# Performance work log

Measured on AMD Instinct MI355X. Metric: run time of the kernel, lower is better.

The kernel has to match this reference:

```python
import jax, jax.numpy as jnp
import numpy as np

B, N, G = 16, 6000, 512
NUM_PAD_GT = 64  # zero-padded gt rows per image


def _make_boxes(key, shape):
    # sample two corner points and sort so (y1,x1) <= (y2,x2)
    r = jax.random.uniform(key, shape[:-1] + (4,), dtype=jnp.float32)
    lo = jnp.minimum(r[..., :2], r[..., 2:])
    hi = jnp.maximum(r[..., :2], r[..., 2:])
    return jnp.concatenate([lo, hi], axis=-1)


def setup_inputs() -> dict:
    key = jax.random.key(0)
    k1, k2, k3 = jax.random.split(key, 3)
    rois = _make_boxes(k1, (B, N, 4))
    gt_boxes = _make_boxes(k2, (B, G, 4))
    # zero-pad tail gt rows (remove_zero_padding signal)
    gt_boxes = gt_boxes.at[:, G - NUM_PAD_GT:, :].set(0.0)
    # ids in [-2, 18]: <0 crowd, ==0 padding, >0 real classes
    gt_ids = jax.random.randint(k3, (B, G), 0, 21, dtype=jnp.int64) - 2
    gt_ids = jnp.where(jnp.arange(G) >= G - NUM_PAD_GT, 0, gt_ids)
    return {"rois": rois, "gt_ids": gt_ids, "gt_boxes": gt_boxes}


def _pairwise_iou(boxes1, boxes2):
    # boxes1: [B,N,4], boxes2: [B,G,4] in (y1,x1,y2,x2) -> IoU [B,N,G]
    b1 = boxes1[:, :, None, :]  # [B,N,1,4]
    b2 = boxes2[:, None, :, :]  # [B,1,G,4]
    y1 = jnp.maximum(b1[..., 0], b2[..., 0])
    x1 = jnp.maximum(b1[..., 1], b2[..., 1])
    y2 = jnp.minimum(b1[..., 2], b2[..., 2])
    x2 = jnp.minimum(b1[..., 3], b2[..., 3])
    inter = jnp.maximum(y2 - y1, 0.0) * jnp.maximum(x2 - x1, 0.0)
    area1 = (b1[..., 2] - b1[..., 0]) * (b1[..., 3] - b1[..., 1])
    area2 = (b2[..., 2] - b2[..., 0]) * (b2[..., 3] - b2[..., 1])
    union = area1 + area2 - inter
    return inter / (union + 1e-8)


def reference(rois, gt_ids, gt_boxes):
    # remove_zero_padding -> validity masks (jit-friendly: mask instead of gather)
    valid_roi = jnp.sum(jnp.abs(rois), axis=-1) > 0.0      # [B,N]
    valid_gt = jnp.sum(jnp.abs(gt_boxes), axis=-1) > 0.0   # [B,G]
    crowd = valid_gt & (gt_ids < 0)                          # [B,G]
    non_crowd = valid_gt & (gt_ids > 0)                      # [B,G]

    iou = _pairwise_iou(rois, gt_boxes)                      # [B,N,G]
    # max IoU against non-crowd / crowd gt subsets (masked cols -> 0, IoU >= 0)
    iou_nc_max = jnp.max(jnp.where(non_crowd[:, None, :], iou, 0.0), axis=2)
    iou_c_max = jnp.max(jnp.where(crowd[:, None, :], iou, 0.0), axis=2)
    iou_nc_max = jnp.where(valid_roi, iou_nc_max, 0.0)       # [B,N]
    iou_c_max = jnp.where(valid_roi, iou_c_max, 0.0)

    positive_mask = valid_roi & (iou_nc_max >= 0.5)
    negative_mask = valid_roi & (iou_nc_max < 0.5) & (iou_c_max < 1e-3)

    iou_maxes = jnp.stack([iou_nc_max, iou_c_max], axis=1)   # [B,2,N]
    return iou_maxes, positive_mask, negative_mask
```

## Files before the change

kernel.cpp:

```cpp
#include <hip/hip_runtime.h>

#define BB 16
#define NN 6000
#define GG 512
#define WAVES 8
#define RPT 3
#define RPB (RPT * 64)

__global__ __launch_bounds__(64 * WAVES) void det_kernel(
    const float4* __restrict__ rois,
    const int*    __restrict__ gt_ids,
    const float4* __restrict__ gt_boxes,
    float*        __restrict__ out)
{
    __shared__ float4 s_box[GG];
    __shared__ float4 s_area4[GG / 4];
    __shared__ float  s_ncm[WAVES][RPB];
    __shared__ float  s_cm[WAVES][RPB];
    __shared__ float  s_val[RPB];
    __shared__ int    s_cnt[2];
    __shared__ int    s_bounds[2];
    float* s_area = (float*)s_area4;

    const int b    = blockIdx.y;
    const int tid  = threadIdx.x;
    const int wave = tid >> 6;
    const int lane = tid & 63;

    if (tid == 0) { s_cnt[0] = 0; s_cnt[1] = 0; }
    __syncthreads();

    {
        const int g = tid;
        float4 box = gt_boxes[b * GG + g];
        float asum = fabsf(box.x) + fabsf(box.y) + fabsf(box.z) + fabsf(box.w);
        int id = gt_ids[b * GG + g];
        const bool pn = (asum > 0.0f) && (id > 0);
        const bool pc = (asum > 0.0f) && (id < 0);
        unsigned long long mn = __ballot(pn);
        unsigned long long mc = __ballot(pc);
        int bn = 0, bc = 0;
        if (lane == 0) {
            bn = atomicAdd(&s_cnt[0], __popcll(mn));
            bc = atomicAdd(&s_cnt[1], __popcll(mc));
        }
        bn = __shfl(bn, 0);
        bc = __shfl(bc, 0);
        const unsigned long long lt = (1ULL << lane) - 1ULL;
        if (pn) {
            int idx = bn + __popcll(mn & lt);
            s_box[idx]  = box;
            s_area[idx] = (box.z - box.x) * (box.w - box.y);
        }
        if (pc) {
            int idx = (GG - 1) - (bc + __popcll(mc & lt));
            s_box[idx]  = box;
            s_area[idx] = (box.z - box.x) * (box.w - box.y);
        }
    }
    __syncthreads();

    if (tid == 0) {
        int ncnt = s_cnt[0];
        int lo   = GG - s_cnt[1];
        int nc_eff = (ncnt + 3) & ~3;
        int lo_pad = lo & ~3;
        if (nc_eff > lo_pad) nc_eff = lo_pad;
        s_bounds[0] = nc_eff;
        s_bounds[1] = lo_pad;
    }
    __syncthreads();

    const int nc_eff = s_bounds[0];
    const int lo_pad = s_bounds[1];

    {
        const float4 z = make_float4(0.f, 0.f, 0.f, 0.f);
        const int ncnt = s_cnt[0];
        const int lo   = GG - s_cnt[1];
        if (tid < 4) {
            int i = ncnt + tid;
            if (i < nc_eff) { s_box[i] = z; s_area[i] = 0.f; }
        } else if (tid < 8) {
            int i = lo_pad + (tid - 4);
            if (i < lo) { s_box[i] = z; s_area[i] = 0.f; }
        }
    }
    __syncthreads();

    const int nbase = blockIdx.x * RPB;
    float4 r[RPT];
    float  rs[RPT];
    #pragma unroll
    for (int i = 0; i < RPT; ++i) {
        int n = nbase + i * 64 + lane;
        float4 rr = (n < NN) ? rois[b * NN + n] : make_float4(0.f, 0.f, 0.f, 0.f);
        r[i]  = rr;
        rs[i] = (rr.z - rr.x) * (rr.w - rr.y) + 1e-8f;
        if (wave == 0)
            s_val[i * 64 + lane] =
                ((fabsf(rr.x) + fabsf(rr.y) + fabsf(rr.z) + fabsf(rr.w)) > 0.f) ? 1.f : 0.f;
    }

    auto tval = [](const float4& rr, float rsum, const float4& g4, float ga) -> float {
        float dy = fminf(rr.z, g4.z) - fmaxf(rr.x, g4.x);
        float dx = fminf(rr.w, g4.w) - fmaxf(rr.y, g4.y);
        float inter = fmaxf(fmaxf(dy, 0.f) * dx, 0.f);
        return inter * __builtin_amdgcn_rcpf(rsum + ga);
    };

    float anc[RPT] = {0.f, 0.f, 0.f};
    float ac[RPT]  = {0.f, 0.f, 0.f};

    {
        const int ngr = nc_eff >> 2;
        const int gpw = (ngr + WAVES - 1) / WAVES;
        const int q0 = wave * gpw;
        const int q1 = min(ngr, q0 + gpw);
        for (int q = q0; q < q1; ++q) {
            float4 b0 = s_box[4 * q + 0];
            float4 b1 = s_box[4 * q + 1];
            float4 b2 = s_box[4 * q + 2];
            float4 b3 = s_box[4 * q + 3];
            float4 a4 = s_area4[q];
            #pragma unroll
            for (int i = 0; i < RPT; ++i) {
                float t0 = tval(r[i], rs[i], b0, a4.x);
                float t1 = tval(r[i], rs[i], b1, a4.y);
                float t2 = tval(r[i], rs[i], b2, a4.z);
                float t3 = tval(r[i], rs[i], b3, a4.w);
                anc[i] = fmaxf(anc[i], fmaxf(fmaxf(t0, t1), fmaxf(t2, t3)));
            }
        }
    }
    {
        const int cg0 = lo_pad >> 2;
        const int cgn = (GG >> 2) - cg0;
        const int gpw = (cgn + WAVES - 1) / WAVES;
        const int q0 = cg0 + wave * gpw;
        const int q1 = min(GG >> 2, q0 + gpw);
        for (int q = q0; q < q1; ++q) {
            float4 b0 = s_box[4 * q + 0];
            float4 b1 = s_box[4 * q + 1];
            float4 b2 = s_box[4 * q + 2];
            float4 b3 = s_box[4 * q + 3];
            float4 a4 = s_area4[q];
            #pragma unroll
            for (int i = 0; i < RPT; ++i) {
                float t0 = tval(r[i], rs[i], b0, a4.x);
                float t1 = tval(r[i], rs[i], b1, a4.y);
                float t2 = tval(r[i], rs[i], b2, a4.z);
                float t3 = tval(r[i], rs[i], b3, a4.w);
                ac[i] = fmaxf(ac[i], fmaxf(fmaxf(t0, t1), fmaxf(t2, t3)));
            }
        }
    }

    #pragma unroll
    for (int i = 0; i < RPT; ++i) {
        s_ncm[wave][i * 64 + lane] = anc[i];
        s_cm[wave][i * 64 + lane]  = ac[i];
    }
    __syncthreads();

    if (tid < RPB) {
        const int n = nbase + tid;
        if (n < NN) {
            float a = s_ncm[0][tid], c = s_cm[0][tid];
            #pragma unroll
            for (int w = 1; w < WAVES; ++w) {
                a = fmaxf(a, s_ncm[w][tid]);
                c = fmaxf(c, s_cm[w][tid]);
            }
            const float vr = s_val[tid];
            a *= vr;
            c *= vr;
            const float nc_max = a * __builtin_amdgcn_rcpf(1.f - a);
            const float c_max  = c * __builtin_amdgcn_rcpf(1.f - c);

            out[b * 2 * NN + n]      = nc_max;
            out[b * 2 * NN + NN + n] = c_max;
            const float pos = (vr > 0.f && nc_max >= 0.5f) ? 1.0f : 0.0f;
            const float neg = (vr > 0.f && nc_max < 0.5f && c_max < 0.001f) ? 1.0f : 0.0f;
            out[BB * 2 * NN + b * NN + n]           = pos;
            out[BB * 2 * NN + BB * NN + b * NN + n] = neg;
        }
    }
}

extern "C" void kernel_launch(void* const* d_in, const int* in_sizes, int n_in,
                              void* d_out, int out_size, void* d_ws, size_t ws_size,
                              hipStream_t stream) {
    const float4* rois     = (const float4*)d_in[0];
    const int*    gt_ids   = (const int*)d_in[1];
    const float4* gt_boxes = (const float4*)d_in[2];
    float*        out      = (float*)d_out;

    dim3 grid((NN + RPB - 1) / RPB, BB);
    det_kernel<<<grid, 64 * WAVES, 0, stream>>>(rois, gt_ids, gt_boxes, out);
}
```

Before: 26.07 us.

## Replace atomic compaction with per-wave prefix counts and software-pipeline LDS box loads

Moves the roi and gt global loads to the top of the kernel so they overlap with each other. The LDS atomic counters and two extra barriers are replaced by per-wave popcounts that every thread prefix-sums. The inner IoU loops become a shared lambda that loads the next gt group from LDS while computing the current one, and the loop bounds are made wave-uniform with readfirstlane. This targets barrier and LDS-latency stalls in a short kernel, at the cost of more live registers, which may reduce occupancy.

```diff
diff --git a/kernel.cpp b/kernel.cpp
--- a/kernel.cpp
+++ b/kernel.cpp
@@ -18,8 +18,7 @@
     __shared__ float  s_ncm[WAVES][RPB];
     __shared__ float  s_cm[WAVES][RPB];
     __shared__ float  s_val[RPB];
-    __shared__ int    s_cnt[2];
-    __shared__ int    s_bounds[2];
+    __shared__ int    s_wn[WAVES], s_wc[WAVES];
     float* s_area = (float*)s_area4;
 
     const int b    = blockIdx.y;
@@ -27,25 +26,46 @@
     const int wave = tid >> 6;
     const int lane = tid & 63;
 
-    if (tid == 0) { s_cnt[0] = 0; s_cnt[1] = 0; }
+    const int nbase = blockIdx.x * RPB;
+    float4 r[RPT];
+    float  rs[RPT];
+    #pragma unroll
+    for (int i = 0; i < RPT; ++i) {
+        int n = nbase + i * 64 + lane;
+        r[i] = (n < NN) ? rois[b * NN + n] : make_float4(0.f, 0.f, 0.f, 0.f);
+    }
+    const float4 box = gt_boxes[b * GG + tid];
+    const int    id  = gt_ids[b * GG + tid];
+
+    #pragma unroll
+    for (int i = 0; i < RPT; ++i) {
+        rs[i] = (r[i].z - r[i].x) * (r[i].w - r[i].y) + 1e-8f;
+        if (wave == 0)
+            s_val[i * 64 + lane] =
+                ((fabsf(r[i].x) + fabsf(r[i].y) + fabsf(r[i].z) + fabsf(r[i].w)) > 0.f) ? 1.f : 0.f;
+    }
+
+    const float asum = fabsf(box.x) + fabsf(box.y) + fabsf(box.z) + fabsf(box.w);
+    const bool pn = (asum > 0.0f) && (id > 0);
+    const bool pc = (asum > 0.0f) && (id < 0);
+    const unsigned long long mn = __ballot(pn);
+    const unsigned long long mc = __ballot(pc);
+    if (lane == 0) { s_wn[wave] = __popcll(mn); s_wc[wave] = __popcll(mc); }
     __syncthreads();
 
+    int bn = 0, bc = 0, ncnt = 0, ccnt = 0;
+    #pragma unroll
+    for (int w = 0; w < WAVES; ++w) {
+        int pw = s_wn[w], cw = s_wc[w];
+        if (w < wave) { bn += pw; bc += cw; }
+        ncnt += pw; ccnt += cw;
+    }
+    const int lo     = GG - ccnt;
+    int nc_eff = (ncnt + 3) & ~3;
+    int lo_pad = lo & ~3;
+    if (nc_eff > lo_pad) nc_eff = lo_pad;
+
     {
-        const int g = tid;
-        float4 box = gt_boxes[b * GG + g];
-        float asum = fabsf(box.x) + fabsf(box.y) + fabsf(box.z) + fabsf(box.w);
-        int id = gt_ids[b * GG + g];
-        const bool pn = (asum > 0.0f) && (id > 0);
-        const bool pc = (asum > 0.0f) && (id < 0);
-        unsigned long long mn = __ballot(pn);
-        unsigned long long mc = __ballot(pc);
-        int bn = 0, bc = 0;
-        if (lane == 0) {
-            bn = atomicAdd(&s_cnt[0], __popcll(mn));
-            bc = atomicAdd(&s_cnt[1], __popcll(mc));
-        }
-        bn = __shfl(bn, 0);
-        bc = __shfl(bc, 0);
         const unsigned long long lt = (1ULL << lane) - 1ULL;
         if (pn) {
             int idx = bn + __popcll(mn & lt);
@@ -57,27 +77,7 @@
             s_box[idx]  = box;
             s_area[idx] = (box.z - box.x) * (box.w - box.y);
         }
-    }
-    __syncthreads();
-
-    if (tid == 0) {
-        int ncnt = s_cnt[0];
-        int lo   = GG - s_cnt[1];
-        int nc_eff = (ncnt + 3) & ~3;
-        int lo_pad = lo & ~3;
-        if (nc_eff > lo_pad) nc_eff = lo_pad;
-        s_bounds[0] = nc_eff;
-        s_bounds[1] = lo_pad;
-    }
-    __syncthreads();
-
-    const int nc_eff = s_bounds[0];
-    const int lo_pad = s_bounds[1];
-
-    {
         const float4 z = make_float4(0.f, 0.f, 0.f, 0.f);
-        const int ncnt = s_cnt[0];
-        const int lo   = GG - s_cnt[1];
         if (tid < 4) {
             int i = ncnt + tid;
             if (i < nc_eff) { s_box[i] = z; s_area[i] = 0.f; }
@@ -87,20 +87,6 @@
         }
     }
     __syncthreads();
-
-    const int nbase = blockIdx.x * RPB;
-    float4 r[RPT];
-    float  rs[RPT];
-    #pragma unroll
-    for (int i = 0; i < RPT; ++i) {
-        int n = nbase + i * 64 + lane;
-        float4 rr = (n < NN) ? rois[b * NN + n] : make_float4(0.f, 0.f, 0.f, 0.f);
-        r[i]  = rr;
-        rs[i] = (rr.z - rr.x) * (rr.w - rr.y) + 1e-8f;
-        if (wave == 0)
-            s_val[i * 64 + lane] =
-                ((fabsf(rr.x) + fabsf(rr.y) + fabsf(rr.z) + fabsf(rr.w)) > 0.f) ? 1.f : 0.f;
-    }
 
     auto tval = [](const float4& rr, float rsum, const float4& g4, float ga) -> float {
         float dy = fminf(rr.z, g4.z) - fmaxf(rr.x, g4.x);
@@ -112,48 +98,47 @@
     float anc[RPT] = {0.f, 0.f, 0.f};
     float ac[RPT]  = {0.f, 0.f, 0.f};
 
+    auto run = [&](int q0, int q1, float* acc) {
+        if (q0 >= q1) return;
+        float4 nb0 = s_box[4 * q0 + 0];
+        float4 nb1 = s_box[4 * q0 + 1];
+        float4 nb2 = s_box[4 * q0 + 2];
+        float4 nb3 = s_box[4 * q0 + 3];
+        float4 na  = s_area4[q0];
+        #pragma unroll 2
+        for (int q = q0; q < q1; ++q) {
+            const float4 cb0 = nb0, cb1 = nb1, cb2 = nb2, cb3 = nb3, ca = na;
+            const int qn = (q + 1 < q1) ? q + 1 : q0;
+            nb0 = s_box[4 * qn + 0];
+            nb1 = s_box[4 * qn + 1];
+            nb2 = s_box[4 * qn + 2];
+            nb3 = s_box[4 * qn + 3];
+            na  = s_area4[qn];
+            #pragma unroll
+            for (int i = 0; i < RPT; ++i) {
+                float t0 = tval(r[i], rs[i], cb0, ca.x);
+                float t1 = tval(r[i], rs[i], cb1, ca.y);
+                float t2 = tval(r[i], rs[i], cb2, ca.z);
+                float t3 = tval(r[i], rs[i], cb3, ca.w);
+                acc[i] = fmaxf(acc[i], fmaxf(fmaxf(t0, t1), fmaxf(t2, t3)));
+            }
+        }
+    };
+
     {
         const int ngr = nc_eff >> 2;
         const int gpw = (ngr + WAVES - 1) / WAVES;
-        const int q0 = wave * gpw;
-        const int q1 = min(ngr, q0 + gpw);
-        for (int q = q0; q < q1; ++q) {
-            float4 b0 = s_box[4 * q + 0];
-            float4 b1 = s_box[4 * q + 1];
-            float4 b2 = s_box[4 * q + 2];
-            float4 b3 = s_box[4 * q + 3];
-            float4 a4 = s_area4[q];
-            #pragma unroll
-            for (int i = 0; i < RPT; ++i) {
-                float t0 = tval(r[i], rs[i], b0, a4.x);
-                float t1 = tval(r[i], rs[i], b1, a4.y);
-                float t2 = tval(r[i], rs[i], b2, a4.z);
-                float t3 = tval(r[i], rs[i], b3, a4.w);
-                anc[i] = fmaxf(anc[i], fmaxf(fmaxf(t0, t1), fmaxf(t2, t3)));
-            }
-        }
+        const int q0 = __builtin_amdgcn_readfirstlane(wave * gpw);
+        const int q1 = __builtin_amdgcn_readfirstlane(min(ngr, q0 + gpw));
+        run(q0, q1, anc);
     }
     {
         const int cg0 = lo_pad >> 2;
         const int cgn = (GG >> 2) - cg0;
         const int gpw = (cgn + WAVES - 1) / WAVES;
-        const int q0 = cg0 + wave * gpw;
-        const int q1 = min(GG >> 2, q0 + gpw);
-        for (int q = q0; q < q1; ++q) {
-            float4 b0 = s_box[4 * q + 0];
-            float4 b1 = s_box[4 * q + 1];
-            float4 b2 = s_box[4 * q + 2];
-            float4 b3 = s_box[4 * q + 3];
-            float4 a4 = s_area4[q];
-            #pragma unroll
-            for (int i = 0; i < RPT; ++i) {
-                float t0 = tval(r[i], rs[i], b0, a4.x);
-                float t1 = tval(r[i], rs[i], b1, a4.y);
-                float t2 = tval(r[i], rs[i], b2, a4.z);
-                float t3 = tval(r[i], rs[i], b3, a4.w);
-                ac[i] = fmaxf(ac[i], fmaxf(fmaxf(t0, t1), fmaxf(t2, t3)));
-            }
-        }
+        const int q0 = __builtin_amdgcn_readfirstlane(cg0 + wave * gpw);
+        const int q1 = __builtin_amdgcn_readfirstlane(min(GG >> 2, q0 + gpw));
+        run(q0, q1, ac);
     }
 
     #pragma unroll
```

After: 23.79 us. -8.7%, faster.
